# Kernel optimization log

Measured on AMD Instinct MI355X. Metric: run time of the kernel, lower is better.

The kernel has to match this reference:

```python
import jax, jax.numpy as jnp
import numpy as np

T, HID = 2048, 1536
H, DK, DV = 12, 128, 128
KEY_DIM, VAL_DIM = H * DK, H * DV
CONV_K, GEN_RED = 4, 8
EPS = 1e-5


def setup_inputs() -> dict:
    key = jax.random.key(0)
    ks = jax.random.split(key, 12)
    def rn(k, sh, scale):
        return jax.random.normal(k, sh, dtype=jnp.float32) * scale
    inv = HID ** -0.5
    return {
        "hidden_states": rn(ks[0], (T, HID), 1.0),
        "Wq": rn(ks[1], (HID, KEY_DIM), inv),
        "Wk": rn(ks[2], (HID, KEY_DIM), inv),
        "Wv": rn(ks[3], (HID, VAL_DIM), inv),
        "Wb": rn(ks[4], (HID, H), inv),
        "Wa": rn(ks[5], (HID, H), inv),
        "A_log": jnp.log(jax.random.uniform(ks[6], (H,), minval=1e-3, maxval=16.0)),
        "dt_bias": jnp.ones((H,), jnp.float32),
        "Wg1": rn(ks[7], (HID, HID // GEN_RED), inv),
        "Wg2": rn(ks[8], (HID // GEN_RED, VAL_DIM * CONV_K), (HID // GEN_RED) ** -0.5),
        "Wgate": rn(ks[9], (HID, VAL_DIM), inv),
        "norm_weight": jnp.ones((DV,), jnp.float32),
        "Wo": rn(ks[10], (VAL_DIM, HID), VAL_DIM ** -0.5),
    }


def _dynamic_conv(v, hs, Wg1, Wg2):
    # per-token per-channel causal depthwise conv; kernels generated from hidden_states
    w = jax.nn.silu(hs @ Wg1) @ Wg2                    # (T, VAL_DIM*K)
    w = w.reshape(T, VAL_DIM, CONV_K)                  # (T, D, K)
    vpad = jnp.pad(v, ((CONV_K - 1, 0), (0, 0)))       # causal left pad
    windows = jnp.stack([vpad[i:i + T] for i in range(CONV_K)], axis=1)  # (T, K, D)
    return jax.nn.silu(jnp.einsum('tkd,tdk->td', windows, w))


def _gated_delta_rule(q, k, v, g, beta):
    # q,k: (T,H,DK); v: (T,H,DV); g,beta: (T,H)
    scale = DK ** -0.5
    def step(S, inp):
        q_t, k_t, v_t, g_t, b_t = inp
        S = S * jnp.exp(g_t)[:, None, None]            # decay state
        kv = jnp.einsum('hk,hkv->hv', k_t, S)          # k^T S
        S = S + jnp.einsum('hk,hv->hkv', k_t, (v_t - kv) * b_t[:, None])
        o_t = jnp.einsum('hk,hkv->hv', q_t, S) * scale
        return S, o_t
    S0 = jnp.zeros((H, DK, DV), jnp.float32)
    _, o = jax.lax.scan(step, S0, (q, k, v, g, beta))
    return o                                           # (T, H, DV)


def reference(hidden_states, Wq, Wk, Wv, Wb, Wa, A_log, dt_bias,
              Wg1, Wg2, Wgate, norm_weight, Wo):
    hs = hidden_states
    q = jax.nn.silu(hs @ Wq).reshape(T, H, DK)
    k = jax.nn.silu(hs @ Wk).reshape(T, H, DK)
    v = _dynamic_conv(hs @ Wv, hs, Wg1, Wg2).reshape(T, H, DV)
    beta = jax.nn.sigmoid(hs @ Wb)                           # (T, H)
    g = -jnp.exp(A_log) * jax.nn.softplus(hs @ Wa + dt_bias)  # (T, H) log-decay
    o = _gated_delta_rule(q, k, v, g, beta)                  # (T, H, DV)
    # gated RMSNorm over head_v_dim
    gate = (hs @ Wgate).reshape(T, H, DV)
    o = o * jax.lax.rsqrt(jnp.mean(o * o, axis=-1, keepdims=True) + EPS)
    o = o * norm_weight * (gate * jax.nn.sigmoid(gate))
    return o.reshape(T, VAL_DIM) @ Wo
```

## Files before the change

kernel.cpp:

```cpp
#include <hip/hip_runtime.h>
#include <hip/hip_bf16.h>
#include <math.h>

#define T     2048
#define HID   1536
#define NH    12
#define DK    128
#define DV    128
#define CONVK 4
#define CH    64
#define NC    32

typedef __attribute__((ext_vector_type(8))) short bf16x8;
typedef __attribute__((ext_vector_type(8))) _Float16 fp16x8;
typedef __attribute__((ext_vector_type(4))) float floatx4;

__device__ __forceinline__ float siluf(float x) {
    return x / (1.0f + __expf(-x));
}
__device__ __forceinline__ unsigned short f2bf(float f) {
    union { __hip_bfloat16 b; unsigned short u; } cv;
    cv.b = __float2bfloat16(f);
    return cv.u;
}
__device__ __forceinline__ float bf2f(unsigned short u) {
    union { unsigned int u; float f; } cv;
    cv.u = ((unsigned int)u) << 16;
    return cv.f;
}
__device__ __forceinline__ unsigned short f2h(float f) {
    union { _Float16 h; unsigned short u; } cv;
    cv.h = (_Float16)f;
    return cv.u;
}
__device__ __forceinline__ void gl_lds16(const void* g, void* l) {
    __builtin_amdgcn_global_load_lds(
        (const __attribute__((address_space(1))) void*)g,
        (__attribute__((address_space(3))) void*)l, 16, 0, 0);
}
__device__ __forceinline__ void split8_store(const float* xv,
                                             unsigned short* dh, unsigned short* dl) {
    ushort4 h0, h1, l0, l1;
    h0.x = f2bf(xv[0]); l0.x = f2bf(xv[0] - bf2f(h0.x));
    h0.y = f2bf(xv[1]); l0.y = f2bf(xv[1] - bf2f(h0.y));
    h0.z = f2bf(xv[2]); l0.z = f2bf(xv[2] - bf2f(h0.z));
    h0.w = f2bf(xv[3]); l0.w = f2bf(xv[3] - bf2f(h0.w));
    h1.x = f2bf(xv[4]); l1.x = f2bf(xv[4] - bf2f(h1.x));
    h1.y = f2bf(xv[5]); l1.y = f2bf(xv[5] - bf2f(h1.y));
    h1.z = f2bf(xv[6]); l1.z = f2bf(xv[6] - bf2f(h1.z));
    h1.w = f2bf(xv[7]); l1.w = f2bf(xv[7] - bf2f(h1.w));
    *(ushort4*)dh = h0; *(ushort4*)(dh + 4) = h1;
    *(ushort4*)dl = l0; *(ushort4*)(dl + 4) = l1;
}

__device__ __forceinline__ void tch_body(const float* __restrict__ src,
                                         unsigned short* __restrict__ dst,
                                         int K, int N, int gx, int gy, int tid,
                                         float* tile ) {
    const int tx = tid & 31, ty = tid >> 5;
    const int k0 = gy * 32, n0 = gx * 32;
#pragma unroll
    for (int r = 0; r < 4; ++r) {
        int kk = k0 + ty + 8 * r, nn = n0 + tx;
        tile[(ty + 8 * r) * 33 + tx] = (nn < N) ? src[(size_t)kk * N + nn] : 0.0f;
    }
    __syncthreads();
#pragma unroll
    for (int r = 0; r < 4; ++r) {
        int nn = n0 + ty + 8 * r, kk = k0 + tx;
        if (nn < N) dst[(size_t)nn * K + kk] = f2h(tile[tx * 33 + ty + 8 * r]);
    }
}
__device__ __forceinline__ void tsp_body(const float* __restrict__ src,
                                         unsigned short* __restrict__ hi,
                                         unsigned short* __restrict__ lo,
                                         int K, int N, int gx, int gy, int tid,
                                         float* tile) {
    const int tx = tid & 31, ty = tid >> 5;
    const int k0 = gy * 32, n0 = gx * 32;
#pragma unroll
    for (int r = 0; r < 4; ++r) {
        int kk = k0 + ty + 8 * r, nn = n0 + tx;
        tile[(ty + 8 * r) * 33 + tx] = (nn < N) ? src[(size_t)kk * N + nn] : 0.0f;
    }
    __syncthreads();
#pragma unroll
    for (int r = 0; r < 4; ++r) {
        int nn = n0 + ty + 8 * r, kk = k0 + tx;
        if (nn < N) {
            float x = tile[tx * 33 + ty + 8 * r];
            unsigned short h = f2bf(x);
            hi[(size_t)nn * K + kk] = h;
            lo[(size_t)nn * K + kk] = f2bf(x - bf2f(h));
        }
    }
}

__global__ __launch_bounds__(256) void prep_all(
    const float* __restrict__ hs,
    unsigned short* __restrict__ hsbh, unsigned short* __restrict__ hsbl,
    unsigned short* __restrict__ hsh,
    const float* __restrict__ Wq, const float* __restrict__ Wv,
    const float* __restrict__ Wgate, const float* __restrict__ Wg1,
    const float* __restrict__ Wg2,
    const float* __restrict__ Wk, const float* __restrict__ Wb,
    const float* __restrict__ Wa,
    unsigned short* __restrict__ WTAfh, unsigned short* __restrict__ WG2h,
    unsigned short* __restrict__ WTBh, unsigned short* __restrict__ WTBl)
{
    __shared__ float tile[32 * 33];
    const int bx = blockIdx.x, tid = threadIdx.x;

    if (bx < 3072) {
        const int i = bx * 256 + tid;
        float4 x = ((const float4*)hs)[i];
        ushort4 h, l, f;
        h.x = f2bf(x.x); l.x = f2bf(x.x - bf2f(h.x)); f.x = f2h(x.x);
        h.y = f2bf(x.y); l.y = f2bf(x.y - bf2f(h.y)); f.y = f2h(x.y);
        h.z = f2bf(x.z); l.z = f2bf(x.z - bf2f(h.z)); f.z = f2h(x.z);
        h.w = f2bf(x.w); l.w = f2bf(x.w - bf2f(h.w)); f.w = f2h(x.w);
        ((ushort4*)hsbh)[i] = h;
        ((ushort4*)hsbl)[i] = l;
        ((ushort4*)hsh)[i]  = f;
    } else if (bx < 5376) {
        const int t = bx - 3072;
        tch_body(Wq, WTAfh, 1536, 1536, t % 48, t / 48, tid, tile);
    } else if (bx < 7680) {
        const int t = bx - 5376;
        tch_body(Wv, WTAfh + 1536 * 1536, 1536, 1536, t % 48, t / 48, tid, tile);
    } else if (bx < 9984) {
        const int t = bx - 7680;
        tch_body(Wgate, WTAfh + 3072 * 1536, 1536, 1536, t % 48, t / 48, tid, tile);
    } else if (bx < 10272) {
        const int t = bx - 9984;
        tch_body(Wg1, WTAfh + 4608 * 1536, 1536, 192, t % 6, t / 6, tid, tile);
    } else if (bx < 11424) {
        const int t = bx - 10272;
        tch_body(Wg2, WG2h, 192, 6144, t % 192, t / 192, tid, tile);
    } else if (bx < 13728) {
        const int t = bx - 11424;
        tsp_body(Wk, WTBh, WTBl, 1536, 1536, t % 48, t / 48, tid, tile);
    } else if (bx < 13776) {
        const int t = bx - 13728;
        tsp_body(Wb, WTBh + 1536 * 1536, WTBl + 1536 * 1536, 1536, 12, 0, t, tid, tile);
    } else {
        const int t = bx - 13776;
        tsp_body(Wa, WTBh + 1548 * 1536, WTBl + 1548 * 1536, 1536, 12, 0, t, tid, tile);
    }
}

__global__ __launch_bounds__(256) void transsplit_kernel(const float* __restrict__ src,
                                                         unsigned short* __restrict__ hi,
                                                         unsigned short* __restrict__ lo,
                                                         int K, int N) {
    __shared__ float tile[32 * 33];
    const int tid = (int)(threadIdx.y * blockDim.x + threadIdx.x);
    tsp_body(src, hi, lo, K, N, blockIdx.x, blockIdx.y, tid, tile);
}

template<int EPI, int MODE>
__global__ __launch_bounds__(256)
void mgemm(const unsigned short* __restrict__ Ah, const unsigned short* __restrict__ Al,
           const unsigned short* __restrict__ Bh, const unsigned short* __restrict__ Bl,
           int K, int N, float* __restrict__ C, unsigned short* __restrict__ Cb)
{
    constexpr int BN   = MODE ? 64 : 128;
    constexpr int BCH  = BN / 16;
    constexpr int NFR  = MODE ? 2 : 4;
    __shared__ unsigned short AsH[2][4096];
    __shared__ unsigned short BsH[2][BCH * 512];
    __shared__ unsigned short AsL[MODE ? 2 : 1][MODE ? 4096 : 4];
    __shared__ unsigned short BsL[MODE ? 2 : 1][MODE ? BCH * 512 : 4];
    const int tid = threadIdx.x;
    const int wave = tid >> 6, lane = tid & 63;
    const int wr = wave >> 1, wc = wave & 1;
    const int lm = lane & 15, lq = lane >> 4;
    const int rowBase = blockIdx.y * 128, colBase = blockIdx.x * BN;

    floatx4 acc[4][NFR];
#pragma unroll
    for (int i = 0; i < 4; ++i)
#pragma unroll
        for (int j = 0; j < NFR; ++j) acc[i][j] = (floatx4){0.f, 0.f, 0.f, 0.f};

    const int mt0 = wave * 2, mt1 = wave * 2 + 1;
    const size_t aOff0 = (size_t)(rowBase + mt0 * 16 + lm) * K + lq * 8;
    const size_t aOff1 = (size_t)(rowBase + mt1 * 16 + lm) * K + lq * 8;
    const size_t bOff0 = (size_t)(colBase + mt0 * 16 + lm) * K + lq * 8;
    const size_t bOff1 = (size_t)(colBase + mt1 * 16 + lm) * K + lq * 8;
    const size_t bOffW = (size_t)(colBase + wave * 16 + lm) * K + lq * 8;

    auto STAGE = [&](int buf, int k0) {
        gl_lds16(Ah + aOff0 + k0, &AsH[buf][mt0 * 512]);
        gl_lds16(Ah + aOff1 + k0, &AsH[buf][mt1 * 512]);
        if (MODE) {
            gl_lds16(Al + aOff0 + k0, &AsL[buf][mt0 * 512]);
            gl_lds16(Al + aOff1 + k0, &AsL[buf][mt1 * 512]);
            gl_lds16(Bh + bOffW + k0, &BsH[buf][wave * 512]);
            gl_lds16(Bl + bOffW + k0, &BsL[buf][wave * 512]);
        } else {
            gl_lds16(Bh + bOff0 + k0, &BsH[buf][mt0 * 512]);
            gl_lds16(Bh + bOff1 + k0, &BsH[buf][mt1 * 512]);
        }
    };

    const int nIter = K >> 5;
    STAGE(0, 0);
    __syncthreads();
    int cur = 0;
    for (int it = 0; it < nIter; ++it) {
        if (it + 1 < nIter) STAGE(cur ^ 1, (it + 1) << 5);
        if (MODE == 0) {
            fp16x8 a[4], b[4];
#pragma unroll
            for (int i = 0; i < 4; ++i) {
                a[i] = *(const fp16x8*)&AsH[cur][(wr * 4 + i) * 512 + lane * 8];
                b[i] = *(const fp16x8*)&BsH[cur][(wc * 4 + i) * 512 + lane * 8];
            }
#pragma unroll
            for (int mi = 0; mi < 4; ++mi)
#pragma unroll
                for (int ni = 0; ni < 4; ++ni)
                    acc[mi][ni] = __builtin_amdgcn_mfma_f32_16x16x32_f16(
                        a[mi], b[ni], acc[mi][ni], 0, 0, 0);
        } else {
            bf16x8 ah[4], al[4], bh[2], bl[2];
#pragma unroll
            for (int i = 0; i < 4; ++i) {
                ah[i] = *(const bf16x8*)&AsH[cur][(wr * 4 + i) * 512 + lane * 8];
                al[i] = *(const bf16x8*)&AsL[cur][(wr * 4 + i) * 512 + lane * 8];
            }
#pragma unroll
            for (int j = 0; j < 2; ++j) {
                bh[j] = *(const bf16x8*)&BsH[cur][(wc * 2 + j) * 512 + lane * 8];
                bl[j] = *(const bf16x8*)&BsL[cur][(wc * 2 + j) * 512 + lane * 8];
            }
#pragma unroll
            for (int mi = 0; mi < 4; ++mi)
#pragma unroll
                for (int ni = 0; ni < 2; ++ni) {
                    acc[mi][ni] = __builtin_amdgcn_mfma_f32_16x16x32_bf16(
                        ah[mi], bh[ni], acc[mi][ni], 0, 0, 0);
                    acc[mi][ni] = __builtin_amdgcn_mfma_f32_16x16x32_bf16(
                        al[mi], bh[ni], acc[mi][ni], 0, 0, 0);
                    acc[mi][ni] = __builtin_amdgcn_mfma_f32_16x16x32_bf16(
                        ah[mi], bl[ni], acc[mi][ni], 0, 0, 0);
                }
        }
        __syncthreads();
        cur ^= 1;
    }

#pragma unroll
    for (int mi = 0; mi < 4; ++mi)
#pragma unroll
        for (int ni = 0; ni < NFR; ++ni) {
            const int col = colBase + wc * (NFR * 16) + ni * 16 + lm;
#pragma unroll
            for (int r = 0; r < 4; ++r) {
                const int row = rowBase + wr * 64 + mi * 16 + lq * 4 + r;
                const float x = acc[mi][ni][r];
                if (EPI == 0) C[(size_t)row * N + col] = x;
                else          Cb[(size_t)row * N + col] = f2bf(x);
            }
        }
}

__global__ __launch_bounds__(256)
void mgemm_ab(const unsigned short* __restrict__ Ah0, const unsigned short* __restrict__ Bh0,
              const unsigned short* __restrict__ Ah1, const unsigned short* __restrict__ Al1,
              const unsigned short* __restrict__ Bh1, const unsigned short* __restrict__ Bl1,
              float* __restrict__ qf, float* __restrict__ vf,
              unsigned short* __restrict__ gsilb, unsigned short* __restrict__ w1h16,
              float* __restrict__ kf,
              const float* __restrict__ A_log, const float* __restrict__ dt_bias,
              float* __restrict__ beta, float* __restrict__ g)
{
    __shared__ unsigned short smem[24576];
    const int tid = threadIdx.x;
    const int wave = tid >> 6, lane = tid & 63;
    const int wr = wave >> 1, wc = wave & 1;
    const int lm = lane & 15, lq = lane >> 4;
    const int K = 1536;
    const int bx = blockIdx.x;

    bool roleA; int aidx = 0, bidx = 0;
    if (bx < 832) { roleA = ((bx & 1) == 0); aidx = bx >> 1; bidx = bx >> 1; }
    else          { roleA = true;            aidx = 416 + (bx - 832); }

    const int mt0 = wave * 2, mt1 = wave * 2 + 1;

    if (roleA) {
        const int rowBase = (aidx / 38) * 128, colBase = (aidx % 38) * 128;
        unsigned short* AsH = smem;
        unsigned short* BsH = smem + 8192;
        floatx4 acc[4][4];
#pragma unroll
        for (int i = 0; i < 4; ++i)
#pragma unroll
            for (int j = 0; j < 4; ++j) acc[i][j] = (floatx4){0.f, 0.f, 0.f, 0.f};

        const size_t aOff0 = (size_t)(rowBase + mt0 * 16 + lm) * K + lq * 8;
        const size_t aOff1 = (size_t)(rowBase + mt1 * 16 + lm) * K + lq * 8;
        const size_t bOff0 = (size_t)(colBase + mt0 * 16 + lm) * K + lq * 8;
        const size_t bOff1 = (size_t)(colBase + mt1 * 16 + lm) * K + lq * 8;

        auto STAGE = [&](int buf, int k0) {
            gl_lds16(Ah0 + aOff0 + k0, &AsH[buf * 4096 + mt0 * 512]);
            gl_lds16(Ah0 + aOff1 + k0, &AsH[buf * 4096 + mt1 * 512]);
            gl_lds16(Bh0 + bOff0 + k0, &BsH[buf * 4096 + mt0 * 512]);
            gl_lds16(Bh0 + bOff1 + k0, &BsH[buf * 4096 + mt1 * 512]);
        };
        STAGE(0, 0);
        __syncthreads();
        int cur = 0;
        for (int it = 0; it < 48; ++it) {
            if (it + 1 < 48) STAGE(cur ^ 1, (it + 1) << 5);
            fp16x8 a[4], b[4];
#pragma unroll
            for (int i = 0; i < 4; ++i) {
                a[i] = *(const fp16x8*)&AsH[cur * 4096 + (wr * 4 + i) * 512 + lane * 8];
                b[i] = *(const fp16x8*)&BsH[cur * 4096 + (wc * 4 + i) * 512 + lane * 8];
            }
#pragma unroll
            for (int mi = 0; mi < 4; ++mi)
#pragma unroll
                for (int ni = 0; ni < 4; ++ni)
                    acc[mi][ni] = __builtin_amdgcn_mfma_f32_16x16x32_f16(
                        a[mi], b[ni], acc[mi][ni], 0, 0, 0);
            __syncthreads();
            cur ^= 1;
        }
#pragma unroll
        for (int mi = 0; mi < 4; ++mi)
#pragma unroll
            for (int ni = 0; ni < 4; ++ni) {
                const int col = colBase + wc * 64 + ni * 16 + lm;
#pragma unroll
                for (int r = 0; r < 4; ++r) {
                    const int row = rowBase + wr * 64 + mi * 16 + lq * 4 + r;
                    const float x = acc[mi][ni][r];
                    if (col < 1536)       qf[(size_t)row * 1536 + col] = siluf(x);
                    else if (col < 3072)  vf[(size_t)row * 1536 + col - 1536] = x;
                    else if (col < 4608)  gsilb[(size_t)row * 1536 + col - 3072] = f2bf(siluf(x));
                    else if (col < 4800)  w1h16[(size_t)row * 192 + col - 4608] = f2h(siluf(x));
                }
            }
    } else {
        const int rowBase = (bidx / 26) * 128, colBase = (bidx % 26) * 64;
        unsigned short* AsH = smem;
        unsigned short* AsL = smem + 8192;
        unsigned short* BsH = smem + 16384;
        unsigned short* BsL = smem + 20480;
        floatx4 acc[4][2];
#pragma unroll
        for (int i = 0; i < 4; ++i)
#pragma unroll
            for (int j = 0; j < 2; ++j) acc[i][j] = (floatx4){0.f, 0.f, 0.f, 0.f};

        const size_t aOff0 = (size_t)(rowBase + mt0 * 16 + lm) * K + lq * 8;
        const size_t aOff1 = (size_t)(rowBase + mt1 * 16 + lm) * K + lq * 8;
        const size_t bOffW = (size_t)(colBase + wave * 16 + lm) * K + lq * 8;

        auto STAGE = [&](int buf, int k0) {
            gl_lds16(Ah1 + aOff0 + k0, &AsH[buf * 4096 + mt0 * 512]);
            gl_lds16(Ah1 + aOff1 + k0, &AsH[buf * 4096 + mt1 * 512]);
            gl_lds16(Al1 + aOff0 + k0, &AsL[buf * 4096 + mt0 * 512]);
            gl_lds16(Al1 + aOff1 + k0, &AsL[buf * 4096 + mt1 * 512]);
            gl_lds16(Bh1 + bOffW + k0, &BsH[buf * 2048 + wave * 512]);
            gl_lds16(Bl1 + bOffW + k0, &BsL[buf * 2048 + wave * 512]);
        };
        STAGE(0, 0);
        __syncthreads();
        int cur = 0;
        for (int it = 0; it < 48; ++it) {
            if (it + 1 < 48) STAGE(cur ^ 1, (it + 1) << 5);
            bf16x8 ah[4], al[4], bh[2], bl[2];
#pragma unroll
            for (int i = 0; i < 4; ++i) {
                ah[i] = *(const bf16x8*)&AsH[cur * 4096 + (wr * 4 + i) * 512 + lane * 8];
                al[i] = *(const bf16x8*)&AsL[cur * 4096 + (wr * 4 + i) * 512 + lane * 8];
            }
#pragma unroll
            for (int j = 0; j < 2; ++j) {
                bh[j] = *(const bf16x8*)&BsH[cur * 2048 + (wc * 2 + j) * 512 + lane * 8];
                bl[j] = *(const bf16x8*)&BsL[cur * 2048 + (wc * 2 + j) * 512 + lane * 8];
            }
#pragma unroll
            for (int mi = 0; mi < 4; ++mi)
#pragma unroll
                for (int ni = 0; ni < 2; ++ni) {
                    acc[mi][ni] = __builtin_amdgcn_mfma_f32_16x16x32_bf16(
                        ah[mi], bh[ni], acc[mi][ni], 0, 0, 0);
                    acc[mi][ni] = __builtin_amdgcn_mfma_f32_16x16x32_bf16(
                        al[mi], bh[ni], acc[mi][ni], 0, 0, 0);
                    acc[mi][ni] = __builtin_amdgcn_mfma_f32_16x16x32_bf16(
                        ah[mi], bl[ni], acc[mi][ni], 0, 0, 0);
                }
            __syncthreads();
            cur ^= 1;
        }
#pragma unroll
        for (int mi = 0; mi < 4; ++mi)
#pragma unroll
            for (int ni = 0; ni < 2; ++ni) {
                const int col = colBase + wc * 32 + ni * 16 + lm;
#pragma unroll
                for (int r = 0; r < 4; ++r) {
                    const int row = rowBase + wr * 64 + mi * 16 + lq * 4 + r;
                    const float x = acc[mi][ni][r];
                    if (col < 1536) {
                        kf[(size_t)row * 1536 + col] = siluf(x);
                    } else if (col < 1560) {
                        const int c2 = col - 1536;
                        if (c2 < 12) {
                            beta[row * NH + c2] = 1.0f / (1.0f + __expf(-x));
                        } else {
                            const int hh = c2 - 12;
                            const float y = x + dt_bias[hh];
                            const float sp = (y > 20.0f) ? y : log1pf(__expf(y));
                            g[row * NH + hh] = -__expf(A_log[hh]) * sp;
                        }
                    }
                }
            }
    }
}

__global__ __launch_bounds__(256)
void convgemm(const unsigned short* __restrict__ Ah, const unsigned short* __restrict__ Bh,
              const float* __restrict__ vpre, float* __restrict__ v)
{
    __shared__ unsigned short smem[16384];
    const int tid = threadIdx.x;
    const int wave = tid >> 6, lane = tid & 63;
    const int wr = wave >> 1, wc = wave & 1;
    const int lm = lane & 15, lq = lane >> 4;
    const int K = 192;
    const int rowBase = blockIdx.y * 128, colBase = blockIdx.x * 128;

    unsigned short* AsH = smem;
    unsigned short* BsH = smem + 8192;

    floatx4 acc[4][4];
#pragma unroll
    for (int i = 0; i < 4; ++i)
#pragma unroll
        for (int j = 0; j < 4; ++j) acc[i][j] = (floatx4){0.f, 0.f, 0.f, 0.f};

    const int mt0 = wave * 2, mt1 = wave * 2 + 1;
    const size_t aOff0 = (size_t)(rowBase + mt0 * 16 + lm) * K + lq * 8;
    const size_t aOff1 = (size_t)(rowBase + mt1 * 16 + lm) * K + lq * 8;
    const size_t bOff0 = (size_t)(colBase + mt0 * 16 + lm) * K + lq * 8;
    const size_t bOff1 = (size_t)(colBase + mt1 * 16 + lm) * K + lq * 8;

    auto STAGE = [&](int buf, int k0) {
        gl_lds16(Ah + aOff0 + k0, &AsH[buf * 4096 + mt0 * 512]);
        gl_lds16(Ah + aOff1 + k0, &AsH[buf * 4096 + mt1 * 512]);
        gl_lds16(Bh + bOff0 + k0, &BsH[buf * 4096 + mt0 * 512]);
        gl_lds16(Bh + bOff1 + k0, &BsH[buf * 4096 + mt1 * 512]);
    };

    const int nIter = 6;
    STAGE(0, 0);
    __syncthreads();
    int cur = 0;
    for (int it = 0; it < nIter; ++it) {
        if (it + 1 < nIter) STAGE(cur ^ 1, (it + 1) << 5);
        fp16x8 a[4], b[4];
#pragma unroll
        for (int i = 0; i < 4; ++i) {
            a[i] = *(const fp16x8*)&AsH[cur * 4096 + (wr * 4 + i) * 512 + lane * 8];
            b[i] = *(const fp16x8*)&BsH[cur * 4096 + (wc * 4 + i) * 512 + lane * 8];
        }
#pragma unroll
        for (int mi = 0; mi < 4; ++mi)
#pragma unroll
            for (int ni = 0; ni < 4; ++ni)
                acc[mi][ni] = __builtin_amdgcn_mfma_f32_16x16x32_f16(
                    a[mi], b[ni], acc[mi][ni], 0, 0, 0);
        __syncthreads();
        cur ^= 1;
    }

#pragma unroll
    for (int mi = 0; mi < 4; ++mi)
#pragma unroll
        for (int ni = 0; ni < 4; ++ni) {
            const int cl = wc * 64 + ni * 16 + lm;
#pragma unroll
            for (int r = 0; r < 4; ++r) {
                const int rl = wr * 64 + mi * 16 + lq * 4 + r;
                smem[rl * 128 + cl] = f2bf(acc[mi][ni][r]);
            }
        }
    __syncthreads();

    const int dB = blockIdx.x * 32;
#pragma unroll
    for (int e = 0; e < 16; ++e) {
        const int u = e * 256 + tid;
        const int tl = u >> 5, dd = u & 31;
        const int t = rowBase + tl, d = dB + dd;
        float a0 = 0.0f;
#pragma unroll
        for (int tap = 0; tap < CONVK; ++tap) {
            const int ts = t - (CONVK - 1) + tap;
            if (ts >= 0)
                a0 += vpre[(size_t)ts * HID + d] * bf2f(smem[tl * 128 + dd * 4 + tap]);
        }
        v[(size_t)t * HID + d] = siluf(a0);
    }
}

__global__ __launch_bounds__(256, 1) void chunkloc_kernel(
    const float* __restrict__ q, const float* __restrict__ k, const float* __restrict__ v,
    const float* __restrict__ g, const float* __restrict__ beta,
    float* __restrict__ X1g,
    unsigned short* __restrict__ X2th, unsigned short* __restrict__ X2tl,
    float* __restrict__ Mg, float* __restrict__ csg,
    unsigned short* __restrict__ Qth, unsigned short* __restrict__ Qtl,
    unsigned short* __restrict__ Kth, unsigned short* __restrict__ Ktl)
{
    __shared__ unsigned short KhS[64 * 136], KlS[64 * 136];
    __shared__ unsigned short QhS[64 * 136], QlS[64 * 136];
    __shared__ float KT[128 * 68];
    __shared__ float Vs[64 * 132];
    __shared__ float As[64 * 68];
    __shared__ float cs[64], sb[64], sbb[64];

    const int c = blockIdx.x, h = blockIdx.y;
    const int tid = threadIdx.x;
    const int wave = tid >> 6, lane = tid & 63;
    const int lm = lane & 15, lq = lane >> 4;
    const int li = tid >> 2, lq4 = tid & 3;
    const size_t rowbase = (size_t)(c * CH) * HID + h * DK;

    {
        const float* ksrc = k + rowbase + (size_t)li * HID + lq4 * 32;
        const float* qsrc = q + rowbase + (size_t)li * HID + lq4 * 32;
        const float* vsrc = v + (size_t)(c * CH + li) * HID + h * DV + lq4 * 32;
#pragma unroll
        for (int f = 0; f < 8; ++f) {
            float4 kx = *(const float4*)(ksrc + f * 4);
            float4 qx = *(const float4*)(qsrc + f * 4);
            float4 vx = *(const float4*)(vsrc + f * 4);
            const int d0 = lq4 * 32 + f * 4;
            {
                ushort4 hh, ll;
                hh.x = f2bf(kx.x); ll.x = f2bf(kx.x - bf2f(hh.x));
                hh.y = f2bf(kx.y); ll.y = f2bf(kx.y - bf2f(hh.y));
                hh.z = f2bf(kx.z); ll.z = f2bf(kx.z - bf2f(hh.z));
                hh.w = f2bf(kx.w); ll.w = f2bf(kx.w - bf2f(hh.w));
                *(ushort4*)&KhS[li * 136 + d0] = hh;
                *(ushort4*)&KlS[li * 136 + d0] = ll;
            }
            {
                ushort4 hh, ll;
                hh.x = f2bf(qx.x); ll.x = f2bf(qx.x - bf2f(hh.x));
                hh.y = f2bf(qx.y); ll.y = f2bf(qx.y - bf2f(hh.y));
                hh.z = f2bf(qx.z); ll.z = f2bf(qx.z - bf2f(hh.z));
                hh.w = f2bf(qx.w); ll.w = f2bf(qx.w - bf2f(hh.w));
                *(ushort4*)&QhS[li * 136 + d0] = hh;
                *(ushort4*)&QlS[li * 136 + d0] = ll;
            }
            KT[(d0 + 0) * 68 + li] = kx.x;
            KT[(d0 + 1) * 68 + li] = kx.y;
            KT[(d0 + 2) * 68 + li] = kx.z;
            KT[(d0 + 3) * 68 + li] = kx.w;
            *(float4*)&Vs[li * 132 + d0] = vx;
        }
    }
    if (tid < 64) {
        float gv = g[(c * CH + tid) * NH + h];
        float bv = beta[(c * CH + tid) * NH + h];
        float csv = gv;
#pragma unroll
        for (int off = 1; off < 64; off <<= 1) {
            float n = __shfl_up(csv, off);
            if (tid >= off) csv += n;
        }
        cs[tid] = csv; sb[tid] = bv; sbb[tid] = bv * __expf(csv);
    }
    __syncthreads();

    {
        const int ti = wave;
#pragma unroll
        for (int tj = 0; tj < 4; ++tj) {
            floatx4 acc = (floatx4){0.f, 0.f, 0.f, 0.f};
#pragma unroll
            for (int ks = 0; ks < 4; ++ks) {
                bf16x8 a_h = *(const bf16x8*)&KhS[(ti * 16 + lm) * 136 + ks * 32 + lq * 8];
                bf16x8 a_l = *(const bf16x8*)&KlS[(ti * 16 + lm) * 136 + ks * 32 + lq * 8];
                bf16x8 b_h = *(const bf16x8*)&KhS[(tj * 16 + lm) * 136 + ks * 32 + lq * 8];
                bf16x8 b_l = *(const bf16x8*)&KlS[(tj * 16 + lm) * 136 + ks * 32 + lq * 8];
                acc = __builtin_amdgcn_mfma_f32_16x16x32_bf16(a_h, b_h, acc, 0, 0, 0);
                acc = __builtin_amdgcn_mfma_f32_16x16x32_bf16(a_h, b_l, acc, 0, 0, 0);
                acc = __builtin_amdgcn_mfma_f32_16x16x32_bf16(a_l, b_h, acc, 0, 0, 0);
            }
#pragma unroll
            for (int r = 0; r < 4; ++r) {
                const int i = ti * 16 + lq * 4 + r, j = tj * 16 + lm;
                As[i * 68 + j] = (j < i) ? sb[i] * __expf(cs[i] - cs[j]) * acc[r] : 0.0f;
            }
        }
        const size_t mbase = (size_t)(h * NC + c) * CH * CH;
#pragma unroll
        for (int tj = 0; tj < 4; ++tj) {
            floatx4 acc = (floatx4){0.f, 0.f, 0.f, 0.f};
#pragma unroll
            for (int ks = 0; ks < 4; ++ks) {
                bf16x8 a_h = *(const bf16x8*)&QhS[(ti * 16 + lm) * 136 + ks * 32 + lq * 8];
                bf16x8 a_l = *(const bf16x8*)&QlS[(ti * 16 + lm) * 136 + ks * 32 + lq * 8];
                bf16x8 b_h = *(const bf16x8*)&KhS[(tj * 16 + lm) * 136 + ks * 32 + lq * 8];
                bf16x8 b_l = *(const bf16x8*)&KlS[(tj * 16 + lm) * 136 + ks * 32 + lq * 8];
                acc = __builtin_amdgcn_mfma_f32_16x16x32_bf16(a_h, b_h, acc, 0, 0, 0);
                acc = __builtin_amdgcn_mfma_f32_16x16x32_bf16(a_h, b_l, acc, 0, 0, 0);
                acc = __builtin_amdgcn_mfma_f32_16x16x32_bf16(a_l, b_h, acc, 0, 0, 0);
            }
#pragma unroll
            for (int r = 0; r < 4; ++r) {
                const int i = ti * 16 + lq * 4 + r, j = tj * 16 + lm;
                Mg[mbase + (size_t)i * 64 + j] =
                    (j <= i) ? __expf(cs[i] - cs[j]) * acc[r] : 0.0f;
            }
        }
    }

    float xc[64];
    const int col = tid;
    if (col < 128) {
#pragma unroll
        for (int i = 0; i < 64; ++i) xc[i] = sb[i] * Vs[i * 132 + col];
    } else {
        const int dcol = col - 128;
#pragma unroll
        for (int i4 = 0; i4 < 16; ++i4) {
            float4 kq = *(const float4*)&KT[dcol * 68 + i4 * 4];
            xc[i4 * 4 + 0] = sbb[i4 * 4 + 0] * kq.x;
            xc[i4 * 4 + 1] = sbb[i4 * 4 + 1] * kq.y;
            xc[i4 * 4 + 2] = sbb[i4 * 4 + 2] * kq.z;
            xc[i4 * 4 + 3] = sbb[i4 * 4 + 3] * kq.w;
        }
    }
    __syncthreads();

#pragma unroll
    for (int i = 1; i < 64; ++i) {
        float a = xc[i];
#pragma unroll
        for (int j4 = 0; j4 < (i + 3) / 4; ++j4) {
            float4 a4 = *(const float4*)&As[i * 68 + j4 * 4];
            a -= a4.x * xc[j4 * 4 + 0] + a4.y * xc[j4 * 4 + 1]
               + a4.z * xc[j4 * 4 + 2] + a4.w * xc[j4 * 4 + 3];
        }
        xc[i] = a;
    }

    {
        const size_t xbase = (size_t)(h * NC + c) * CH * 128;
        if (col < 128) {
            for (int i = 0; i < 64; ++i) X1g[xbase + (size_t)i * 128 + col] = xc[i];
        } else {
            for (int i = 0; i < 64; ++i) Vs[i * 132 + (col - 128)] = xc[i];
        }
    }
    if (tid < 64) csg[(size_t)(h * NC + c) * CH + tid] = cs[tid];
    __syncthreads();

    const size_t tb = (size_t)(h * NC + c) * 8192;

    {
#pragma unroll
        for (int e = 0; e < 4; ++e) {
            int u = e * 256 + tid;
            int ch = u >> 6, l = u & 63;
            int i = (ch >> 2) * 16 + (l & 15);
            int dbase = (ch & 3) * 32 + (l >> 4) * 8;
            float4 a = *(const float4*)&Vs[i * 132 + dbase];
            float4 b = *(const float4*)&Vs[i * 132 + dbase + 4];
            float xv[8] = {-a.x, -a.y, -a.z, -a.w, -b.x, -b.y, -b.z, -b.w};
            split8_store(xv, &X2th[tb + ch * 512 + l * 8], &X2tl[tb + ch * 512 + l * 8]);
        }
    }
    {
#pragma unroll
        for (int e = 0; e < 4; ++e) {
            int u = e * 256 + tid;
            int ch = u >> 6, l = u & 63;
            int i = (ch >> 2) * 16 + (l & 15);
            int dbase = (ch & 3) * 32 + (l >> 4) * 8;
            *(bf16x8*)&Qth[tb + ch * 512 + l * 8] = *(const bf16x8*)&QhS[i * 136 + dbase];
            *(bf16x8*)&Qtl[tb + ch * 512 + l * 8] = *(const bf16x8*)&QlS[i * 136 + dbase];
        }
    }
    {
#pragma unroll
        for (int e = 0; e < 4; ++e) {
            int u = e * 256 + tid;
            int ch = u >> 6, l = u & 63;
            int dk = (ch >> 1) * 16 + (l & 15);
            int ibase = (ch & 1) * 32 + (l >> 4) * 8;
            float4 a = *(const float4*)&KT[dk * 68 + ibase];
            float4 b = *(const float4*)&KT[dk * 68 + ibase + 4];
            float xv[8] = {a.x, a.y, a.z, a.w, b.x, b.y, b.z, b.w};
            split8_store(xv, &Kth[tb + ch * 512 + l * 8], &Ktl[tb + ch * 512 + l * 8]);
        }
    }
}

struct StFrags {
    bf16x8 xh[4], xl[4], qh[4], ql[4], kh[4], kl[4];
    float x1r[4], csr[4], cs63;
};

__device__ __forceinline__ void st_load(
    StFrags& f,
    const unsigned short* __restrict__ Qth, const unsigned short* __restrict__ Qtl,
    const unsigned short* __restrict__ Kth, const unsigned short* __restrict__ Ktl,
    const unsigned short* __restrict__ X2th, const unsigned short* __restrict__ X2tl,
    const float* __restrict__ X1g, const float* __restrict__ csg,
    int h, int c, int db, int mw, int lane, int lq, int lm)
{
    const size_t hc = (size_t)(h * NC + c);
    const size_t xb = hc * CH * 128;
    const size_t tb = hc * 8192 + (size_t)lane * 8;
#pragma unroll
    for (int ks = 0; ks < 4; ++ks) {
        const size_t off = tb + (size_t)(mw * 4 + ks) * 512;
        f.xh[ks] = *(const bf16x8*)(X2th + off);
        f.xl[ks] = *(const bf16x8*)(X2tl + off);
        f.qh[ks] = *(const bf16x8*)(Qth + off);
        f.ql[ks] = *(const bf16x8*)(Qtl + off);
        f.kh[ks] = *(const bf16x8*)(Kth + off);
        f.kl[ks] = *(const bf16x8*)(Ktl + off);
    }
#pragma unroll
    for (int r = 0; r < 4; ++r) {
        const int row = mw * 16 + lq * 4 + r;
        f.x1r[r] = X1g[xb + (size_t)row * 128 + db * 16 + lm];
        f.csr[r] = csg[hc * CH + row];
    }
    f.cs63 = csg[hc * CH + 63];
}

__device__ __forceinline__ void st_compute(
    const StFrags& f, floatx4& st0, floatx4& st1,
    unsigned short* SBh, unsigned short* SBl,
    unsigned short* UBh, unsigned short* UBl,
    float* __restrict__ X1g, float* __restrict__ o,
    int h, int c, int db, int mw, int lane, int lq, int lm)
{
    const size_t hc = (size_t)(h * NC + c);
    const size_t xb = hc * CH * 128;

    {
        floatx4 aU0 = (floatx4){0.f, 0.f, 0.f, 0.f};
        floatx4 aU1 = (floatx4){0.f, 0.f, 0.f, 0.f};
        floatx4 aO0 = (floatx4){0.f, 0.f, 0.f, 0.f};
        floatx4 aO1 = (floatx4){0.f, 0.f, 0.f, 0.f};
#pragma unroll
        for (int ks = 0; ks < 4; ++ks) {
            bf16x8 sh = *(const bf16x8*)&SBh[lm * 136 + ks * 32 + lq * 8];
            bf16x8 sl = *(const bf16x8*)&SBl[lm * 136 + ks * 32 + lq * 8];
            if (ks & 1) {
                aU1 = __builtin_amdgcn_mfma_f32_16x16x32_bf16(f.xh[ks], sh, aU1, 0, 0, 0);
                aU1 = __builtin_amdgcn_mfma_f32_16x16x32_bf16(f.xh[ks], sl, aU1, 0, 0, 0);
                aU1 = __builtin_amdgcn_mfma_f32_16x16x32_bf16(f.xl[ks], sh, aU1, 0, 0, 0);
                aO1 = __builtin_amdgcn_mfma_f32_16x16x32_bf16(f.qh[ks], sh, aO1, 0, 0, 0);
                aO1 = __builtin_amdgcn_mfma_f32_16x16x32_bf16(f.qh[ks], sl, aO1, 0, 0, 0);
                aO1 = __builtin_amdgcn_mfma_f32_16x16x32_bf16(f.ql[ks], sh, aO1, 0, 0, 0);
            } else {
                aU0 = __builtin_amdgcn_mfma_f32_16x16x32_bf16(f.xh[ks], sh, aU0, 0, 0, 0);
                aU0 = __builtin_amdgcn_mfma_f32_16x16x32_bf16(f.xh[ks], sl, aU0, 0, 0, 0);
                aU0 = __builtin_amdgcn_mfma_f32_16x16x32_bf16(f.xl[ks], sh, aU0, 0, 0, 0);
                aO0 = __builtin_amdgcn_mfma_f32_16x16x32_bf16(f.qh[ks], sh, aO0, 0, 0, 0);
                aO0 = __builtin_amdgcn_mfma_f32_16x16x32_bf16(f.qh[ks], sl, aO0, 0, 0, 0);
                aO0 = __builtin_amdgcn_mfma_f32_16x16x32_bf16(f.ql[ks], sh, aO0, 0, 0, 0);
            }
        }
#pragma unroll
        for (int r = 0; r < 4; ++r) {
            const int row = mw * 16 + lq * 4 + r;
            const float u = aU0[r] + aU1[r] + f.x1r[r];
            X1g[xb + (size_t)row * 128 + db * 16 + lm] = u;
            const float up = u * __expf(f.cs63 - f.csr[r]);
            unsigned short uh = f2bf(up);
            UBh[lm * 72 + row] = uh;
            UBl[lm * 72 + row] = f2bf(up - bf2f(uh));
            o[(size_t)(c * CH + row) * HID + h * DV + db * 16 + lm] =
                __expf(f.csr[r]) * (aO0[r] + aO1[r]);
        }
    }
    __syncthreads();

    {
        const float bC = __expf(f.cs63);
#pragma unroll
        for (int mt2 = 0; mt2 < 2; ++mt2) {
            const int mt = mw * 2 + mt2;
            floatx4 acc;
            floatx4 stc = mt2 ? st1 : st0;
#pragma unroll
            for (int r = 0; r < 4; ++r) acc[r] = bC * stc[r];
#pragma unroll
            for (int ks = 0; ks < 2; ++ks) {
                bf16x8 ah = f.kh[mt2 * 2 + ks];
                bf16x8 al = f.kl[mt2 * 2 + ks];
                bf16x8 bh = *(const bf16x8*)&UBh[lm * 72 + ks * 32 + lq * 8];
                bf16x8 bl = *(const bf16x8*)&UBl[lm * 72 + ks * 32 + lq * 8];
                acc = __builtin_amdgcn_mfma_f32_16x16x32_bf16(ah, bh, acc, 0, 0, 0);
                acc = __builtin_amdgcn_mfma_f32_16x16x32_bf16(ah, bl, acc, 0, 0, 0);
                acc = __builtin_amdgcn_mfma_f32_16x16x32_bf16(al, bh, acc, 0, 0, 0);
            }
            if (mt2) st1 = acc; else st0 = acc;
            ushort4 shv, slv;
#pragma unroll
            for (int r = 0; r < 4; ++r) {
                const float sv = acc[r];
                unsigned short sh = f2bf(sv);
                ((unsigned short*)&shv)[r] = sh;
                ((unsigned short*)&slv)[r] = f2bf(sv - bf2f(sh));
            }
            const int dkb = mt * 16 + lq * 4;
            *(ushort4*)&SBh[lm * 136 + dkb] = shv;
            *(ushort4*)&SBl[lm * 136 + dkb] = slv;
        }
    }
    __syncthreads();
}

__global__ __launch_bounds__(256, 1) void state_kernel(
    const unsigned short* __restrict__ Qth, const unsigned short* __restrict__ Qtl,
    const unsigned short* __restrict__ Kth, const unsigned short* __restrict__ Ktl,
    const unsigned short* __restrict__ X2th, const unsigned short* __restrict__ X2tl,
    float* __restrict__ X1g, const float* __restrict__ csg, float* __restrict__ o)
{
    __shared__ unsigned short SBh[16 * 136], SBl[16 * 136];
    __shared__ unsigned short UBh[16 * 72],  UBl[16 * 72];

    const int h = blockIdx.x, db = blockIdx.y;
    const int tid = threadIdx.x;
    const int mw = tid >> 6, lane = tid & 63;
    const int lm = lane & 15, lq = lane >> 4;

    for (int idx = tid; idx < 16 * 136; idx += 256) { SBh[idx] = 0; SBl[idx] = 0; }
    floatx4 st0 = (floatx4){0.f, 0.f, 0.f, 0.f};
    floatx4 st1 = (floatx4){0.f, 0.f, 0.f, 0.f};
    __syncthreads();

    StFrags fA, fB;
    st_load(fA, Qth, Qtl, Kth, Ktl, X2th, X2tl, X1g, csg, h, 0, db, mw, lane, lq, lm);
    for (int c = 0; c < NC; c += 2) {
        st_load(fB, Qth, Qtl, Kth, Ktl, X2th, X2tl, X1g, csg, h, c + 1, db, mw, lane, lq, lm);
        __builtin_amdgcn_sched_barrier(0);
        st_compute(fA, st0, st1, SBh, SBl, UBh, UBl, X1g, o, h, c, db, mw, lane, lq, lm);
        if (c + 2 < NC)
            st_load(fA, Qth, Qtl, Kth, Ktl, X2th, X2tl, X1g, csg, h, c + 2, db, mw, lane, lq, lm);
        __builtin_amdgcn_sched_barrier(0);
        st_compute(fB, st0, st1, SBh, SBl, UBh, UBl, X1g, o, h, c + 1, db, mw, lane, lq, lm);
    }
}

__global__ __launch_bounds__(256) void outknorm_kernel(
    const float* __restrict__ Ug, const float* __restrict__ Mg,
    const float* __restrict__ o ,
    const unsigned short* __restrict__ gsil, const float* __restrict__ nw,
    unsigned short* __restrict__ out_hi, unsigned short* __restrict__ out_lo)
{
    __shared__ float Msh[64 * 68];
    __shared__ float Ush[64 * 132];
    __shared__ float rsq[64];

    const int c = blockIdx.x, h = blockIdx.y;
    const int tid = threadIdx.x;
    const size_t hc = (size_t)(h * NC + c);

    for (int e = 0; e < 16; ++e) {
        int idx = e * 256 + tid;
        Msh[(idx >> 6) * 68 + (idx & 63)] = Mg[hc * CH * CH + idx];
    }
    for (int e = 0; e < 32; ++e) {
        int idx = e * 256 + tid;
        int j = idx >> 7, cc = idx & 127;
        Ush[j * 132 + cc] = Ug[hc * CH * 128 + (size_t)j * 128 + cc];
    }
    __syncthreads();

    const int tx = tid & 15, ty = tid >> 4;
    const int c0 = tx * 8, i0 = ty * 4;
    float acc[4][8] = {{0}};
    for (int j4 = 0; j4 < 16; ++j4) {
        float uv[4][8];
#pragma unroll
        for (int s = 0; s < 4; ++s) {
            float4 u4a = *(const float4*)&Ush[(j4 * 4 + s) * 132 + c0];
            float4 u4b = *(const float4*)&Ush[(j4 * 4 + s) * 132 + c0 + 4];
            uv[s][0] = u4a.x; uv[s][1] = u4a.y; uv[s][2] = u4a.z; uv[s][3] = u4a.w;
            uv[s][4] = u4b.x; uv[s][5] = u4b.y; uv[s][6] = u4b.z; uv[s][7] = u4b.w;
        }
#pragma unroll
        for (int r = 0; r < 4; ++r) {
            float4 m4 = *(const float4*)&Msh[(i0 + r) * 68 + j4 * 4];
            const float mv[4] = {m4.x, m4.y, m4.z, m4.w};
#pragma unroll
            for (int s = 0; s < 4; ++s)
#pragma unroll
                for (int e = 0; e < 8; ++e) acc[r][e] += mv[s] * uv[s][e];
        }
    }
    __syncthreads();

    const float scale = 0.08838834764831845f;
#pragma unroll
    for (int r = 0; r < 4; ++r) {
        const float* op = &o[(size_t)(c * CH + i0 + r) * HID + h * DV + c0];
        float4 p0 = *(const float4*)op;
        float4 p1 = *(const float4*)(op + 4);
        const float pv[8] = {p0.x, p0.y, p0.z, p0.w, p1.x, p1.y, p1.z, p1.w};
#pragma unroll
        for (int e = 0; e < 8; ++e)
            Ush[(i0 + r) * 132 + c0 + e] = scale * (pv[e] + acc[r][e]);
    }
    __syncthreads();

    {
        const int row = tid >> 2, sub = tid & 3;
        float ss = 0.0f;
#pragma unroll
        for (int k2 = 0; k2 < 32; ++k2) {
            float x = Ush[row * 132 + sub * 32 + k2];
            ss += x * x;
        }
        ss += __shfl_xor(ss, 1);
        ss += __shfl_xor(ss, 2);
        if (sub == 0) rsq[row] = rsqrtf(ss * (1.0f / 128.0f) + 1e-5f);
    }
    __syncthreads();

    for (int e = 0; e < 32; ++e) {
        int idx = e * 256 + tid;
        int j = idx >> 7, cc = idx & 127;
        const size_t base = (size_t)(c * CH + j) * HID + h * DV;
        float va = Ush[j * 132 + cc] * rsq[j] * nw[cc] * bf2f(gsil[base + cc]);
        unsigned short ha = f2bf(va);
        out_hi[base + cc] = ha;
        out_lo[base + cc] = f2bf(va - bf2f(ha));
    }
}

extern "C" void kernel_launch(void* const* d_in, const int* in_sizes, int n_in,
                              void* d_out, int out_size, void* d_ws, size_t ws_size,
                              hipStream_t stream) {
    const float* hs      = (const float*)d_in[0];
    const float* Wq      = (const float*)d_in[1];
    const float* Wk      = (const float*)d_in[2];
    const float* Wv      = (const float*)d_in[3];
    const float* Wb      = (const float*)d_in[4];
    const float* Wa      = (const float*)d_in[5];
    const float* A_log   = (const float*)d_in[6];
    const float* dt_bias = (const float*)d_in[7];
    const float* Wg1     = (const float*)d_in[8];
    const float* Wg2     = (const float*)d_in[9];
    const float* Wgate   = (const float*)d_in[10];
    const float* norm_w  = (const float*)d_in[11];
    const float* Wo      = (const float*)d_in[12];

    float* ws = (float*)d_ws;
    float* q    = ws;
    float* kbuf = ws + 3145728;
    float* vpre = ws + 6291456;
    float* vbuf = ws + 9437184;
    unsigned short* gsil = (unsigned short*)(ws + 12582912);
    float* X1g  = ws + 14155776;
    unsigned short* X2th = (unsigned short*)(ws + 17301504);
    unsigned short* X2tl = (unsigned short*)(ws + 18874368);
    float* Mg   = ws + 20447232;
    unsigned short* WTAfh = (unsigned short*)(ws + 14155776);
    unsigned short* WTBh  = (unsigned short*)(ws + 17891328);
    unsigned short* WTBl  = (unsigned short*)(ws + 19169280);
    unsigned short* WG2h  = (unsigned short*)(ws + 22044672);
    unsigned short* hsh   = (unsigned short*)(ws + 22634496);
    unsigned short* w1h16 = (unsigned short*)(ws + 24207360);
    unsigned short* Kth = (unsigned short*)(ws + 22044672);
    unsigned short* Ktl = (unsigned short*)(ws + 23617536);
    float* beta  = ws + 25190400;
    float* g     = ws + 25214976;
    float* csg   = ws + 25239552;
    unsigned short* hsbh = (unsigned short*)(ws + 9437184);
    unsigned short* hsbl = (unsigned short*)(ws + 11010048);
    unsigned short* Qth  = (unsigned short*)(ws + 6291456);
    unsigned short* Qtl  = (unsigned short*)(ws + 7864320);
    unsigned short* WoTh = (unsigned short*)(ws);
    unsigned short* WoTl = (unsigned short*)(ws + 1179648);
    unsigned short* onh  = (unsigned short*)(ws + 6291456);
    unsigned short* onl  = (unsigned short*)(ws + 7864320);

    const dim3 blk(256);

    prep_all<<<13824, blk, 0, stream>>>(hs, hsbh, hsbl, hsh,
                                        Wq, Wv, Wgate, Wg1, Wg2, Wk, Wb, Wa,
                                        WTAfh, WG2h, WTBh, WTBl);

    mgemm_ab<<<1024, blk, 0, stream>>>(hsh, WTAfh, hsbh, hsbl, WTBh, WTBl,
                                       q, vpre, gsil, w1h16, kbuf,
                                       A_log, dt_bias, beta, g);

    convgemm<<<dim3(48, 16), blk, 0, stream>>>(w1h16, WG2h, vpre, vbuf);

    chunkloc_kernel<<<dim3(NC, NH), blk, 0, stream>>>(q, kbuf, vbuf, g, beta,
                                                      X1g, X2th, X2tl, Mg, csg,
                                                      Qth, Qtl, Kth, Ktl);
    state_kernel<<<dim3(NH, 8), blk, 0, stream>>>(Qth, Qtl, Kth, Ktl, X2th, X2tl,
                                                  X1g, csg, vbuf);
    transsplit_kernel<<<dim3(48, 48), blk, 0, stream>>>(Wo, WoTh, WoTl, 1536, 1536);

    outknorm_kernel<<<dim3(NC, NH), blk, 0, stream>>>(X1g, Mg, vbuf, gsil, norm_w,
                                                      onh, onl);
    mgemm<0, 1><<<dim3(24, 16), blk, 0, stream>>>(onh, onl, WoTh, WoTl, 1536, 1536,
        (float*)d_out, nullptr);
}
```

Baseline: 532.4 us.

## Use single fp16 operands for output projection and deepen GEMM K-stages

The output projection GEMM drops the bf16 hi/lo split (three MFMAs per tile step) and instead uses single fp16 operands for both the normalized activations and the transposed Wo, via a new fgemm kernel. The Wo transpose kernel now emits only one fp16 half. Both fgemm and the role-A path of mgemm_ab stage 64 K-elements per pipeline step instead of 32, halving barrier count at the cost of doubled LDS. This cuts MFMA work and memory traffic for the final GEMM but lowers precision to fp16, risking overflow or accuracy loss.

```diff
diff --git a/kernel.cpp b/kernel.cpp
--- a/kernel.cpp
+++ b/kernel.cpp
@@ -149,121 +149,11 @@
     }
 }
 
-__global__ __launch_bounds__(256) void transsplit_kernel(const float* __restrict__ src,
-                                                         unsigned short* __restrict__ hi,
-                                                         unsigned short* __restrict__ lo,
+__global__ __launch_bounds__(256) void transcasth_kernel(const float* __restrict__ src,
+                                                         unsigned short* __restrict__ dst,
                                                          int K, int N) {
     __shared__ float tile[32 * 33];
-    const int tid = (int)(threadIdx.y * blockDim.x + threadIdx.x);
-    tsp_body(src, hi, lo, K, N, blockIdx.x, blockIdx.y, tid, tile);
-}
-
-template<int EPI, int MODE>
-__global__ __launch_bounds__(256)
-void mgemm(const unsigned short* __restrict__ Ah, const unsigned short* __restrict__ Al,
-           const unsigned short* __restrict__ Bh, const unsigned short* __restrict__ Bl,
-           int K, int N, float* __restrict__ C, unsigned short* __restrict__ Cb)
-{
-    constexpr int BN   = MODE ? 64 : 128;
-    constexpr int BCH  = BN / 16;
-    constexpr int NFR  = MODE ? 2 : 4;
-    __shared__ unsigned short AsH[2][4096];
-    __shared__ unsigned short BsH[2][BCH * 512];
-    __shared__ unsigned short AsL[MODE ? 2 : 1][MODE ? 4096 : 4];
-    __shared__ unsigned short BsL[MODE ? 2 : 1][MODE ? BCH * 512 : 4];
-    const int tid = threadIdx.x;
-    const int wave = tid >> 6, lane = tid & 63;
-    const int wr = wave >> 1, wc = wave & 1;
-    const int lm = lane & 15, lq = lane >> 4;
-    const int rowBase = blockIdx.y * 128, colBase = blockIdx.x * BN;
-
-    floatx4 acc[4][NFR];
-#pragma unroll
-    for (int i = 0; i < 4; ++i)
-#pragma unroll
-        for (int j = 0; j < NFR; ++j) acc[i][j] = (floatx4){0.f, 0.f, 0.f, 0.f};
-
-    const int mt0 = wave * 2, mt1 = wave * 2 + 1;
-    const size_t aOff0 = (size_t)(rowBase + mt0 * 16 + lm) * K + lq * 8;
-    const size_t aOff1 = (size_t)(rowBase + mt1 * 16 + lm) * K + lq * 8;
-    const size_t bOff0 = (size_t)(colBase + mt0 * 16 + lm) * K + lq * 8;
-    const size_t bOff1 = (size_t)(colBase + mt1 * 16 + lm) * K + lq * 8;
-    const size_t bOffW = (size_t)(colBase + wave * 16 + lm) * K + lq * 8;
-
-    auto STAGE = [&](int buf, int k0) {
-        gl_lds16(Ah + aOff0 + k0, &AsH[buf][mt0 * 512]);
-        gl_lds16(Ah + aOff1 + k0, &AsH[buf][mt1 * 512]);
-        if (MODE) {
-            gl_lds16(Al + aOff0 + k0, &AsL[buf][mt0 * 512]);
-            gl_lds16(Al + aOff1 + k0, &AsL[buf][mt1 * 512]);
-            gl_lds16(Bh + bOffW + k0, &BsH[buf][wave * 512]);
-            gl_lds16(Bl + bOffW + k0, &BsL[buf][wave * 512]);
-        } else {
-            gl_lds16(Bh + bOff0 + k0, &BsH[buf][mt0 * 512]);
-            gl_lds16(Bh + bOff1 + k0, &BsH[buf][mt1 * 512]);
-        }
-    };
-
-    const int nIter = K >> 5;
-    STAGE(0, 0);
-    __syncthreads();
-    int cur = 0;
-    for (int it = 0; it < nIter; ++it) {
-        if (it + 1 < nIter) STAGE(cur ^ 1, (it + 1) << 5);
-        if (MODE == 0) {
-            fp16x8 a[4], b[4];
-#pragma unroll
-            for (int i = 0; i < 4; ++i) {
-                a[i] = *(const fp16x8*)&AsH[cur][(wr * 4 + i) * 512 + lane * 8];
-                b[i] = *(const fp16x8*)&BsH[cur][(wc * 4 + i) * 512 + lane * 8];
-            }
-#pragma unroll
-            for (int mi = 0; mi < 4; ++mi)
-#pragma unroll
-                for (int ni = 0; ni < 4; ++ni)
-                    acc[mi][ni] = __builtin_amdgcn_mfma_f32_16x16x32_f16(
-                        a[mi], b[ni], acc[mi][ni], 0, 0, 0);
-        } else {
-            bf16x8 ah[4], al[4], bh[2], bl[2];
-#pragma unroll
-            for (int i = 0; i < 4; ++i) {
-                ah[i] = *(const bf16x8*)&AsH[cur][(wr * 4 + i) * 512 + lane * 8];
-                al[i] = *(const bf16x8*)&AsL[cur][(wr * 4 + i) * 512 + lane * 8];
-            }
-#pragma unroll
-            for (int j = 0; j < 2; ++j) {
-                bh[j] = *(const bf16x8*)&BsH[cur][(wc * 2 + j) * 512 + lane * 8];
-                bl[j] = *(const bf16x8*)&BsL[cur][(wc * 2 + j) * 512 + lane * 8];
-            }
-#pragma unroll
-            for (int mi = 0; mi < 4; ++mi)
-#pragma unroll
-                for (int ni = 0; ni < 2; ++ni) {
-                    acc[mi][ni] = __builtin_amdgcn_mfma_f32_16x16x32_bf16(
-                        ah[mi], bh[ni], acc[mi][ni], 0, 0, 0);
-                    acc[mi][ni] = __builtin_amdgcn_mfma_f32_16x16x32_bf16(
-                        al[mi], bh[ni], acc[mi][ni], 0, 0, 0);
-                    acc[mi][ni] = __builtin_amdgcn_mfma_f32_16x16x32_bf16(
-                        ah[mi], bl[ni], acc[mi][ni], 0, 0, 0);
-                }
-        }
-        __syncthreads();
-        cur ^= 1;
-    }
-
-#pragma unroll
-    for (int mi = 0; mi < 4; ++mi)
-#pragma unroll
-        for (int ni = 0; ni < NFR; ++ni) {
-            const int col = colBase + wc * (NFR * 16) + ni * 16 + lm;
-#pragma unroll
-            for (int r = 0; r < 4; ++r) {
-                const int row = rowBase + wr * 64 + mi * 16 + lq * 4 + r;
-                const float x = acc[mi][ni][r];
-                if (EPI == 0) C[(size_t)row * N + col] = x;
-                else          Cb[(size_t)row * N + col] = f2bf(x);
-            }
-        }
+    tch_body(src, dst, K, N, blockIdx.x, blockIdx.y, threadIdx.x, tile);
 }
 
 __global__ __launch_bounds__(256)
@@ -276,7 +166,7 @@
               const float* __restrict__ A_log, const float* __restrict__ dt_bias,
               float* __restrict__ beta, float* __restrict__ g)
 {
-    __shared__ unsigned short smem[24576];
+    __shared__ unsigned short smem[32768];
     const int tid = threadIdx.x;
     const int wave = tid >> 6, lane = tid & 63;
     const int wr = wave >> 1, wc = wave & 1;
@@ -293,7 +183,7 @@
     if (roleA) {
         const int rowBase = (aidx / 38) * 128, colBase = (aidx % 38) * 128;
         unsigned short* AsH = smem;
-        unsigned short* BsH = smem + 8192;
+        unsigned short* BsH = smem + 16384;
         floatx4 acc[4][4];
 #pragma unroll
         for (int i = 0; i < 4; ++i)
@@ -306,28 +196,35 @@
         const size_t bOff1 = (size_t)(colBase + mt1 * 16 + lm) * K + lq * 8;
 
         auto STAGE = [&](int buf, int k0) {
-            gl_lds16(Ah0 + aOff0 + k0, &AsH[buf * 4096 + mt0 * 512]);
-            gl_lds16(Ah0 + aOff1 + k0, &AsH[buf * 4096 + mt1 * 512]);
-            gl_lds16(Bh0 + bOff0 + k0, &BsH[buf * 4096 + mt0 * 512]);
-            gl_lds16(Bh0 + bOff1 + k0, &BsH[buf * 4096 + mt1 * 512]);
+            gl_lds16(Ah0 + aOff0 + k0,      &AsH[buf * 8192 + mt0 * 512]);
+            gl_lds16(Ah0 + aOff1 + k0,      &AsH[buf * 8192 + mt1 * 512]);
+            gl_lds16(Ah0 + aOff0 + k0 + 32, &AsH[buf * 8192 + 4096 + mt0 * 512]);
+            gl_lds16(Ah0 + aOff1 + k0 + 32, &AsH[buf * 8192 + 4096 + mt1 * 512]);
+            gl_lds16(Bh0 + bOff0 + k0,      &BsH[buf * 8192 + mt0 * 512]);
+            gl_lds16(Bh0 + bOff1 + k0,      &BsH[buf * 8192 + mt1 * 512]);
+            gl_lds16(Bh0 + bOff0 + k0 + 32, &BsH[buf * 8192 + 4096 + mt0 * 512]);
+            gl_lds16(Bh0 + bOff1 + k0 + 32, &BsH[buf * 8192 + 4096 + mt1 * 512]);
         };
         STAGE(0, 0);
         __syncthreads();
         int cur = 0;
-        for (int it = 0; it < 48; ++it) {
-            if (it + 1 < 48) STAGE(cur ^ 1, (it + 1) << 5);
-            fp16x8 a[4], b[4];
-#pragma unroll
-            for (int i = 0; i < 4; ++i) {
-                a[i] = *(const fp16x8*)&AsH[cur * 4096 + (wr * 4 + i) * 512 + lane * 8];
-                b[i] = *(const fp16x8*)&BsH[cur * 4096 + (wc * 4 + i) * 512 + lane * 8];
-            }
-#pragma unroll
-            for (int mi = 0; mi < 4; ++mi)
-#pragma unroll
-                for (int ni = 0; ni < 4; ++ni)
-                    acc[mi][ni] = __builtin_amdgcn_mfma_f32_16x16x32_f16(
-                        a[mi], b[ni], acc[mi][ni], 0, 0, 0);
+        for (int it = 0; it < 24; ++it) {
+            if (it + 1 < 24) STAGE(cur ^ 1, (it + 1) << 6);
+#pragma unroll
+            for (int s = 0; s < 2; ++s) {
+                fp16x8 a[4], b[4];
+#pragma unroll
+                for (int i = 0; i < 4; ++i) {
+                    a[i] = *(const fp16x8*)&AsH[cur * 8192 + s * 4096 + (wr * 4 + i) * 512 + lane * 8];
+                    b[i] = *(const fp16x8*)&BsH[cur * 8192 + s * 4096 + (wc * 4 + i) * 512 + lane * 8];
+                }
+#pragma unroll
+                for (int mi = 0; mi < 4; ++mi)
+#pragma unroll
+                    for (int ni = 0; ni < 4; ++ni)
+                        acc[mi][ni] = __builtin_amdgcn_mfma_f32_16x16x32_f16(
+                            a[mi], b[ni], acc[mi][ni], 0, 0, 0);
+            }
             __syncthreads();
             cur ^= 1;
         }
@@ -428,6 +325,77 @@
 }
 
 __global__ __launch_bounds__(256)
+void fgemm(const unsigned short* __restrict__ Ah, const unsigned short* __restrict__ Bh,
+           float* __restrict__ C)
+{
+    __shared__ unsigned short AsH[2][8192];
+    __shared__ unsigned short BsH[2][4096];
+    const int tid = threadIdx.x;
+    const int wave = tid >> 6, lane = tid & 63;
+    const int wr = wave >> 1, wc = wave & 1;
+    const int lm = lane & 15, lq = lane >> 4;
+    const int K = 1536;
+    const int rowBase = blockIdx.y * 128, colBase = blockIdx.x * 64;
+
+    floatx4 acc[4][2];
+#pragma unroll
+    for (int i = 0; i < 4; ++i)
+#pragma unroll
+        for (int j = 0; j < 2; ++j) acc[i][j] = (floatx4){0.f, 0.f, 0.f, 0.f};
+
+    const int mt0 = wave * 2, mt1 = wave * 2 + 1;
+    const size_t aOff0 = (size_t)(rowBase + mt0 * 16 + lm) * K + lq * 8;
+    const size_t aOff1 = (size_t)(rowBase + mt1 * 16 + lm) * K + lq * 8;
+    const size_t bOffW = (size_t)(colBase + wave * 16 + lm) * K + lq * 8;
+
+    auto STAGE = [&](int buf, int k0) {
+        gl_lds16(Ah + aOff0 + k0,      &AsH[buf][mt0 * 512]);
+        gl_lds16(Ah + aOff1 + k0,      &AsH[buf][mt1 * 512]);
+        gl_lds16(Ah + aOff0 + k0 + 32, &AsH[buf][4096 + mt0 * 512]);
+        gl_lds16(Ah + aOff1 + k0 + 32, &AsH[buf][4096 + mt1 * 512]);
+        gl_lds16(Bh + bOffW + k0,      &BsH[buf][wave * 512]);
+        gl_lds16(Bh + bOffW + k0 + 32, &BsH[buf][2048 + wave * 512]);
+    };
+
+    STAGE(0, 0);
+    __syncthreads();
+    int cur = 0;
+    for (int it = 0; it < 24; ++it) {
+        if (it + 1 < 24) STAGE(cur ^ 1, (it + 1) << 6);
+#pragma unroll
+        for (int s = 0; s < 2; ++s) {
+            fp16x8 a[4], b[2];
+#pragma unroll
+            for (int i = 0; i < 4; ++i)
+                a[i] = *(const fp16x8*)&AsH[cur][s * 4096 + (wr * 4 + i) * 512 + lane * 8];
+#pragma unroll
+            for (int j = 0; j < 2; ++j)
+                b[j] = *(const fp16x8*)&BsH[cur][s * 2048 + (wc * 2 + j) * 512 + lane * 8];
+#pragma unroll
+            for (int mi = 0; mi < 4; ++mi)
+#pragma unroll
+                for (int ni = 0; ni < 2; ++ni)
+                    acc[mi][ni] = __builtin_amdgcn_mfma_f32_16x16x32_f16(
+                        a[mi], b[ni], acc[mi][ni], 0, 0, 0);
+        }
+        __syncthreads();
+        cur ^= 1;
+    }
+
+#pragma unroll
+    for (int mi = 0; mi < 4; ++mi)
+#pragma unroll
+        for (int ni = 0; ni < 2; ++ni) {
+            const int col = colBase + wc * 32 + ni * 16 + lm;
+#pragma unroll
+            for (int r = 0; r < 4; ++r) {
+                const int row = rowBase + wr * 64 + mi * 16 + lq * 4 + r;
+                C[(size_t)row * 1536 + col] = acc[mi][ni][r];
+            }
+        }
+}
+
+__global__ __launch_bounds__(256)
 void convgemm(const unsigned short* __restrict__ Ah, const unsigned short* __restrict__ Bh,
               const float* __restrict__ vpre, float* __restrict__ v)
 {
@@ -867,7 +835,7 @@
     const float* __restrict__ Ug, const float* __restrict__ Mg,
     const float* __restrict__ o ,
     const unsigned short* __restrict__ gsil, const float* __restrict__ nw,
-    unsigned short* __restrict__ out_hi, unsigned short* __restrict__ out_lo)
+    unsigned short* __restrict__ out_h)
 {
     __shared__ float Msh[64 * 68];
     __shared__ float Ush[64 * 132];
@@ -944,9 +912,7 @@
         int j = idx >> 7, cc = idx & 127;
         const size_t base = (size_t)(c * CH + j) * HID + h * DV;
         float va = Ush[j * 132 + cc] * rsq[j] * nw[cc] * bf2f(gsil[base + cc]);
-        unsigned short ha = f2bf(va);
-        out_hi[base + cc] = ha;
-        out_lo[base + cc] = f2bf(va - bf2f(ha));
+        out_h[base + cc] = f2h(va);
     }
 }
 
@@ -993,9 +959,7 @@
     unsigned short* Qth  = (unsigned short*)(ws + 6291456);
     unsigned short* Qtl  = (unsigned short*)(ws + 7864320);
     unsigned short* WoTh = (unsigned short*)(ws);
-    unsigned short* WoTl = (unsigned short*)(ws + 1179648);
     unsigned short* onh  = (unsigned short*)(ws + 6291456);
-    unsigned short* onl  = (unsigned short*)(ws + 7864320);
 
     const dim3 blk(256);
 
@@ -1014,10 +978,8 @@
                                                       Qth, Qtl, Kth, Ktl);
     state_kernel<<<dim3(NH, 8), blk, 0, stream>>>(Qth, Qtl, Kth, Ktl, X2th, X2tl,
                                                   X1g, csg, vbuf);
-    transsplit_kernel<<<dim3(48, 48), blk, 0, stream>>>(Wo, WoTh, WoTl, 1536, 1536);
-
-    outknorm_kernel<<<dim3(NC, NH), blk, 0, stream>>>(X1g, Mg, vbuf, gsil, norm_w,
-                                                      onh, onl);
-    mgemm<0, 1><<<dim3(24, 16), blk, 0, stream>>>(onh, onl, WoTh, WoTl, 1536, 1536,
-        (float*)d_out, nullptr);
-}
+    transcasth_kernel<<<dim3(48, 48), blk, 0, stream>>>(Wo, WoTh, 1536, 1536);
+
+    outknorm_kernel<<<dim3(NC, NH), blk, 0, stream>>>(X1g, Mg, vbuf, gsil, norm_w, onh);
+    fgemm<<<dim3(24, 16), blk, 0, stream>>>(onh, WoTh, (float*)d_out);
+}
```

Result: faster. 498.7 us (-6.3%).
